# Performance work log

Measured on AMD Instinct MI355X. Metric: run time of the kernel, lower is better.

## Reference

```python
import jax, jax.numpy as jnp
import numpy as np

# RReLU in eval mode is leaky_relu with slope = (lower+upper)/2 = (1/8 + 1/3)/2
RRELU_SLOPE = (1.0 / 8.0 + 1.0 / 3.0) / 2.0  # = 11/48

N_NODES, FEAT_DIM = 100000, 512
EMBED_DIM = 256
BATCH, NUM_SAMPLE = 16384, 10


def setup_inputs() -> dict:
    key = jax.random.key(0)
    k1, k2, k3 = jax.random.split(key, 3)
    features = jax.random.normal(k1, (N_NODES, FEAT_DIM), dtype=jnp.float32)
    # Xavier-uniform-style init for the weight [embed_dim, feat_dim]
    bound = float(np.sqrt(6.0 / (EMBED_DIM + FEAT_DIM)))
    weight = jax.random.uniform(k2, (EMBED_DIM, FEAT_DIM), dtype=jnp.float32,
                                minval=-bound, maxval=bound)
    # Pre-sampled neighbor ids per batch node: [BATCH, NUM_SAMPLE]
    neigh_idx = jax.random.randint(k3, (BATCH, NUM_SAMPLE), 0, N_NODES, dtype=jnp.int64)
    return {"features": features, "weight": weight, "neigh_idx": neigh_idx}


def reference(features, weight, neigh_idx):
    # Mean aggregator: gather sampled neighbor features and average -> [B, F]
    agg = jnp.take(features, neigh_idx, axis=0).mean(axis=1)
    # weight.mm(agg.t()) -> [E, B]
    y = jnp.einsum("ef,bf->eb", weight, agg)
    # RReLU (eval mode): leaky with mean slope
    return jnp.where(y >= 0, y, y * RRELU_SLOPE)
```

## Files before the change

### kernel.cpp

```cpp
#include <hip/hip_runtime.h>
#include <stdint.h>

constexpr int FEAT  = 512;
constexpr int EMB   = 256;
constexpr int BATCH = 16384;
constexpr int NSAMP = 10;
constexpr float SLOPE  = 11.0f / 48.0f;
constexpr float INV_NS = 1.0f / 10.0f;

using f32x4  = __attribute__((ext_vector_type(4))) float;
using frag8  = __attribute__((ext_vector_type(8))) short;

static __device__ __forceinline__ ushort f2b(float x) {
    unsigned u = __builtin_bit_cast(unsigned, x);
    unsigned r = (u + 0x7fffu + ((u >> 16) & 1u)) >> 16;
    return (ushort)r;
}

__global__ __launch_bounds__(256) void agg_kernel(const float* __restrict__ feat,
                                                  const int*   __restrict__ idx,
                                                  ushort*      __restrict__ aggb) {
    int t = blockIdx.x * 256 + threadIdx.x;
    int b = t >> 7;
    int c = (t & 127) << 2;
    const int* ib = idx + b * NSAMP;
    float sx = 0.f, sy = 0.f, sz = 0.f, sw = 0.f;
#pragma unroll
    for (int j = 0; j < NSAMP; ++j) {
        long n = ib[j];
        const float4 v = *reinterpret_cast<const float4*>(feat + n * FEAT + c);
        sx += v.x; sy += v.y; sz += v.z; sw += v.w;
    }
    ushort4 o;
    o.x = f2b(sx * INV_NS); o.y = f2b(sy * INV_NS);
    o.z = f2b(sz * INV_NS); o.w = f2b(sw * INV_NS);
    *reinterpret_cast<ushort4*>(aggb + (size_t)b * FEAT + c) = o;
}

__global__ __launch_bounds__(256) void w2b_kernel(const float* __restrict__ w,
                                                  ushort*      __restrict__ wb) {
    int t = blockIdx.x * 256 + threadIdx.x;
    const float4 v = *reinterpret_cast<const float4*>(w + (size_t)t * 4);
    ushort4 o;
    o.x = f2b(v.x); o.y = f2b(v.y); o.z = f2b(v.z); o.w = f2b(v.w);
    *reinterpret_cast<ushort4*>(wb + (size_t)t * 4) = o;
}

__global__ __launch_bounds__(256) void gemm_kernel(const ushort* __restrict__ Wb,
                                                   const ushort* __restrict__ Ab,
                                                   float*        __restrict__ out) {
    __shared__ ushort As[128 * 32];
    __shared__ ushort Bs[128 * 32];

    const int tid  = threadIdx.x;
    const int m0   = blockIdx.y * 128;
    const int n0   = blockIdx.x * 128;
    const int w    = tid >> 6;
    const int lane = tid & 63;
    const int wr   = w >> 1, wc = w & 1;
    const int l15  = lane & 15, lq = lane >> 4;

    f32x4 acc[4][4] = {};

    for (int k0 = 0; k0 < FEAT; k0 += 32) {
#pragma unroll
        for (int cc = 0; cc < 2; ++cc) {
            int o  = cc * 4096 + tid * 16;
            int r  = o >> 6;
            int kk = (o & 63) >> 1;
            __builtin_amdgcn_global_load_lds(
                (const __attribute__((address_space(1))) void*)(Wb + (size_t)(m0 + r) * FEAT + k0 + kk),
                (__attribute__((address_space(3))) void*)((char*)As + o), 16, 0, 0);
            __builtin_amdgcn_global_load_lds(
                (const __attribute__((address_space(1))) void*)(Ab + (size_t)(n0 + r) * FEAT + k0 + kk),
                (__attribute__((address_space(3))) void*)((char*)Bs + o), 16, 0, 0);
        }
        __syncthreads();

        frag8 af[4], bf[4];
#pragma unroll
        for (int i = 0; i < 4; ++i)
            af[i] = *reinterpret_cast<const frag8*>(&As[(wr * 64 + i * 16 + l15) * 32 + lq * 8]);
#pragma unroll
        for (int j = 0; j < 4; ++j)
            bf[j] = *reinterpret_cast<const frag8*>(&Bs[(wc * 64 + j * 16 + l15) * 32 + lq * 8]);

#pragma unroll
        for (int i = 0; i < 4; ++i)
#pragma unroll
            for (int j = 0; j < 4; ++j)
                acc[i][j] = __builtin_amdgcn_mfma_f32_16x16x32_bf16(af[i], bf[j], acc[i][j], 0, 0, 0);
        __syncthreads();
    }

#pragma unroll
    for (int i = 0; i < 4; ++i) {
        int row_base = m0 + wr * 64 + i * 16 + lq * 4;
#pragma unroll
        for (int j = 0; j < 4; ++j) {
            int col = n0 + wc * 64 + j * 16 + l15;
#pragma unroll
            for (int q = 0; q < 4; ++q) {
                float y = acc[i][j][q];
                y = (y >= 0.f) ? y : y * SLOPE;
                out[(size_t)(row_base + q) * BATCH + col] = y;
            }
        }
    }
}

__global__ __launch_bounds__(256) void fused_fallback(const float* __restrict__ feat,
                                                      const float* __restrict__ w,
                                                      const int*   __restrict__ idx,
                                                      float*       __restrict__ out) {
    __shared__ float agg[FEAT];
    int b = blockIdx.x;
    const int* ib = idx + b * NSAMP;
    for (int c = threadIdx.x; c < FEAT; c += 256) {
        float s = 0.f;
        for (int j = 0; j < NSAMP; ++j) s += feat[(long)ib[j] * FEAT + c];
        agg[c] = s * INV_NS;
    }
    __syncthreads();
    int e = threadIdx.x;
    float a = 0.f;
    const float* wr = w + (size_t)e * FEAT;
    for (int f = 0; f < FEAT; ++f) a += wr[f] * agg[f];
    out[(size_t)e * BATCH + b] = (a >= 0.f) ? a : a * SLOPE;
}

extern "C" void kernel_launch(void* const* d_in, const int* in_sizes, int n_in,
                              void* d_out, int out_size, void* d_ws, size_t ws_size,
                              hipStream_t stream) {
    const float* feat = (const float*)d_in[0];
    const float* wgt  = (const float*)d_in[1];
    const int*   idx  = (const int*)d_in[2];
    float*       out  = (float*)d_out;

    const size_t agg_elems = (size_t)BATCH * FEAT;
    const size_t w_elems   = (size_t)EMB * FEAT;
    const size_t need      = (agg_elems + w_elems) * sizeof(ushort);

    if (ws_size >= need) {
        ushort* aggb = (ushort*)d_ws;
        ushort* wb   = aggb + agg_elems;
        agg_kernel<<<(BATCH * FEAT / 4) / 256, 256, 0, stream>>>(feat, idx, aggb);
        w2b_kernel<<<(EMB * FEAT / 4) / 256, 256, 0, stream>>>(wgt, wb);
        dim3 grid(BATCH / 128, EMB / 128);
        gemm_kernel<<<grid, 256, 0, stream>>>(wb, aggb, out);
    } else {
        fused_fallback<<<BATCH, 256, 0, stream>>>(feat, wgt, idx, out);
    }
}
```

Baseline: 69.52 us.

## Fuse gather-mean aggregation and bf16 GEMM into a single kernel

Replaces the three-kernel pipeline (aggregate to bf16 workspace, convert weights, tiled GEMM) with one kernel per 32-row batch tile. The kernel gathers and averages neighbor features into swizzled LDS, then streams fp32 weights from global memory, converting them to bf16 in registers for MFMA. This removes the intermediate workspace round-trip and the extra launches. In exchange, every block re-reads the full weight matrix through cache. The workspace-size fallback path is also removed.

After: 75.90 us. 9.2% more time.

```diff
diff --git a/kernel.cpp b/kernel.cpp
--- a/kernel.cpp
+++ b/kernel.cpp
@@ -5,128 +5,106 @@
 constexpr int EMB   = 256;
 constexpr int BATCH = 16384;
 constexpr int NSAMP = 10;
+constexpr int NB    = 32;
 constexpr float SLOPE  = 11.0f / 48.0f;
 constexpr float INV_NS = 1.0f / 10.0f;
 
-using f32x4  = __attribute__((ext_vector_type(4))) float;
-using frag8  = __attribute__((ext_vector_type(8))) short;
+using f32x4 = __attribute__((ext_vector_type(4))) float;
+using frag8 = __attribute__((ext_vector_type(8))) short;
 
-static __device__ __forceinline__ ushort f2b(float x) {
+static __device__ __forceinline__ unsigned f2b(float x) {
     unsigned u = __builtin_bit_cast(unsigned, x);
-    unsigned r = (u + 0x7fffu + ((u >> 16) & 1u)) >> 16;
-    return (ushort)r;
+    return (u + 0x7fffu + ((u >> 16) & 1u)) >> 16;
+}
+static __device__ __forceinline__ unsigned pk2(float lo, float hi) {
+    return f2b(lo) | (f2b(hi) << 16);
 }
 
-__global__ __launch_bounds__(256) void agg_kernel(const float* __restrict__ feat,
-                                                  const int*   __restrict__ idx,
-                                                  ushort*      __restrict__ aggb) {
-    int t = blockIdx.x * 256 + threadIdx.x;
-    int b = t >> 7;
-    int c = (t & 127) << 2;
-    const int* ib = idx + b * NSAMP;
-    float sx = 0.f, sy = 0.f, sz = 0.f, sw = 0.f;
+__global__ __launch_bounds__(256, 2) void enc_fused(const float* __restrict__ feat,
+                                                    const float* __restrict__ wgt,
+                                                    const int*   __restrict__ idx,
+                                                    float*       __restrict__ out) {
+    __shared__ ushort Bs[NB * FEAT];
+
+    const int tid = threadIdx.x;
+    const int n0  = blockIdx.x * NB;
+
+    {
+        const int r   = tid >> 3;
+        const int sub = tid & 7;
+        const int* ib = idx + (size_t)(n0 + r) * NSAMP;
+        const float* base[NSAMP];
 #pragma unroll
-    for (int j = 0; j < NSAMP; ++j) {
-        long n = ib[j];
-        const float4 v = *reinterpret_cast<const float4*>(feat + n * FEAT + c);
-        sx += v.x; sy += v.y; sz += v.z; sw += v.w;
+        for (int j = 0; j < NSAMP; ++j)
+            base[j] = feat + (size_t)ib[j] * FEAT;
+        const int swz = (r & 7) << 4;
+#pragma unroll
+        for (int c = 0; c < 16; ++c) {
+            const int col4 = c * 8 + sub;
+            float sx = 0.f, sy = 0.f, sz = 0.f, sw = 0.f;
+#pragma unroll
+            for (int j = 0; j < NSAMP; ++j) {
+                const float4 v = *reinterpret_cast<const float4*>(base[j] + col4 * 4);
+                sx += v.x; sy += v.y; sz += v.z; sw += v.w;
+            }
+            ushort4 o;
+            o.x = (ushort)f2b(sx * INV_NS); o.y = (ushort)f2b(sy * INV_NS);
+            o.z = (ushort)f2b(sz * INV_NS); o.w = (ushort)f2b(sw * INV_NS);
+            const int kb = (col4 * 8) ^ swz;
+            *reinterpret_cast<ushort4*>((char*)Bs + r * (FEAT * 2) + kb) = o;
+        }
     }
-    ushort4 o;
-    o.x = f2b(sx * INV_NS); o.y = f2b(sy * INV_NS);
-    o.z = f2b(sz * INV_NS); o.w = f2b(sw * INV_NS);
-    *reinterpret_cast<ushort4*>(aggb + (size_t)b * FEAT + c) = o;
-}
+    __syncthreads();
 
-__global__ __launch_bounds__(256) void w2b_kernel(const float* __restrict__ w,
-                                                  ushort*      __restrict__ wb) {
-    int t = blockIdx.x * 256 + threadIdx.x;
-    const float4 v = *reinterpret_cast<const float4*>(w + (size_t)t * 4);
-    ushort4 o;
-    o.x = f2b(v.x); o.y = f2b(v.y); o.z = f2b(v.z); o.w = f2b(v.w);
-    *reinterpret_cast<ushort4*>(wb + (size_t)t * 4) = o;
-}
+    const int wv   = tid >> 6;
+    const int lane = tid & 63;
+    const int l15  = lane & 15, lq = lane >> 4;
+    const int mb   = wv * 64;
 
-__global__ __launch_bounds__(256) void gemm_kernel(const ushort* __restrict__ Wb,
-                                                   const ushort* __restrict__ Ab,
-                                                   float*        __restrict__ out) {
-    __shared__ ushort As[128 * 32];
-    __shared__ ushort Bs[128 * 32];
+    f32x4 acc[4][2] = {};
 
-    const int tid  = threadIdx.x;
-    const int m0   = blockIdx.y * 128;
-    const int n0   = blockIdx.x * 128;
-    const int w    = tid >> 6;
-    const int lane = tid & 63;
-    const int wr   = w >> 1, wc = w & 1;
-    const int l15  = lane & 15, lq = lane >> 4;
-
-    f32x4 acc[4][4] = {};
-
+#pragma unroll
     for (int k0 = 0; k0 < FEAT; k0 += 32) {
+        frag8 af[4], bf[2];
 #pragma unroll
-        for (int cc = 0; cc < 2; ++cc) {
-            int o  = cc * 4096 + tid * 16;
-            int r  = o >> 6;
-            int kk = (o & 63) >> 1;
-            __builtin_amdgcn_global_load_lds(
-                (const __attribute__((address_space(1))) void*)(Wb + (size_t)(m0 + r) * FEAT + k0 + kk),
-                (__attribute__((address_space(3))) void*)((char*)As + o), 16, 0, 0);
-            __builtin_amdgcn_global_load_lds(
-                (const __attribute__((address_space(1))) void*)(Ab + (size_t)(n0 + r) * FEAT + k0 + kk),
-                (__attribute__((address_space(3))) void*)((char*)Bs + o), 16, 0, 0);
+        for (int i = 0; i < 4; ++i) {
+            const float* wp = wgt + (size_t)(mb + i * 16 + l15) * FEAT + k0 + lq * 8;
+            const float4 a0 = *reinterpret_cast<const float4*>(wp);
+            const float4 a1 = *reinterpret_cast<const float4*>(wp + 4);
+            union { frag8 f; unsigned u[4]; } pk;
+            pk.u[0] = pk2(a0.x, a0.y);
+            pk.u[1] = pk2(a0.z, a0.w);
+            pk.u[2] = pk2(a1.x, a1.y);
+            pk.u[3] = pk2(a1.z, a1.w);
+            af[i] = pk.f;
         }
-        __syncthreads();
-
-        frag8 af[4], bf[4];
 #pragma unroll
-        for (int i = 0; i < 4; ++i)
-            af[i] = *reinterpret_cast<const frag8*>(&As[(wr * 64 + i * 16 + l15) * 32 + lq * 8]);
-#pragma unroll
-        for (int j = 0; j < 4; ++j)
-            bf[j] = *reinterpret_cast<const frag8*>(&Bs[(wc * 64 + j * 16 + l15) * 32 + lq * 8]);
-
+        for (int j = 0; j < 2; ++j) {
+            const int row = j * 16 + l15;
+            const int kb  = (k0 * 2 + lq * 16) ^ ((row & 7) << 4);
+            bf[j] = *reinterpret_cast<const frag8*>((const char*)Bs + row * (FEAT * 2) + kb);
+        }
 #pragma unroll
         for (int i = 0; i < 4; ++i)
 #pragma unroll
-            for (int j = 0; j < 4; ++j)
+            for (int j = 0; j < 2; ++j)
                 acc[i][j] = __builtin_amdgcn_mfma_f32_16x16x32_bf16(af[i], bf[j], acc[i][j], 0, 0, 0);
-        __syncthreads();
     }
 
 #pragma unroll
     for (int i = 0; i < 4; ++i) {
-        int row_base = m0 + wr * 64 + i * 16 + lq * 4;
+        const int rb = mb + i * 16 + lq * 4;
 #pragma unroll
-        for (int j = 0; j < 4; ++j) {
-            int col = n0 + wc * 64 + j * 16 + l15;
+        for (int j = 0; j < 2; ++j) {
+            const int col = n0 + j * 16 + l15;
 #pragma unroll
             for (int q = 0; q < 4; ++q) {
                 float y = acc[i][j][q];
                 y = (y >= 0.f) ? y : y * SLOPE;
-                out[(size_t)(row_base + q) * BATCH + col] = y;
+                out[(size_t)(rb + q) * BATCH + col] = y;
             }
         }
     }
-}
-
-__global__ __launch_bounds__(256) void fused_fallback(const float* __restrict__ feat,
-                                                      const float* __restrict__ w,
-                                                      const int*   __restrict__ idx,
-                                                      float*       __restrict__ out) {
-    __shared__ float agg[FEAT];
-    int b = blockIdx.x;
-    const int* ib = idx + b * NSAMP;
-    for (int c = threadIdx.x; c < FEAT; c += 256) {
-        float s = 0.f;
-        for (int j = 0; j < NSAMP; ++j) s += feat[(long)ib[j] * FEAT + c];
-        agg[c] = s * INV_NS;
-    }
-    __syncthreads();
-    int e = threadIdx.x;
-    float a = 0.f;
-    const float* wr = w + (size_t)e * FEAT;
-    for (int f = 0; f < FEAT; ++f) a += wr[f] * agg[f];
-    out[(size_t)e * BATCH + b] = (a >= 0.f) ? a : a * SLOPE;
 }
 
 extern "C" void kernel_launch(void* const* d_in, const int* in_sizes, int n_in,
@@ -137,18 +115,5 @@
     const int*   idx  = (const int*)d_in[2];
     float*       out  = (float*)d_out;
 
-    const size_t agg_elems = (size_t)BATCH * FEAT;
-    const size_t w_elems   = (size_t)EMB * FEAT;
-    const size_t need      = (agg_elems + w_elems) * sizeof(ushort);
-
-    if (ws_size >= need) {
-        ushort* aggb = (ushort*)d_ws;
-        ushort* wb   = aggb + agg_elems;
-        agg_kernel<<<(BATCH * FEAT / 4) / 256, 256, 0, stream>>>(feat, idx, aggb);
-        w2b_kernel<<<(EMB * FEAT / 4) / 256, 256, 0, stream>>>(wgt, wb);
-        dim3 grid(BATCH / 128, EMB / 128);
-        gemm_kernel<<<grid, 256, 0, stream>>>(wb, aggb, out);
-    } else {
-        fused_fallback<<<BATCH, 256, 0, stream>>>(feat, wgt, idx, out);
-    }
+    enc_fused<<<BATCH / NB, 256, 0, stream>>>(feat, wgt, idx, out);
 }
```
